# Kernel tuning notes

Measured on AMD Instinct MI355X. Metric: run time of the kernel, lower is better.

The kernel has to match this reference:

```python
import jax, jax.numpy as jnp
from jax import lax
import numpy as np

KSIZE = 3        # matching kernel size
RATE = 2         # downsample rate; raw kernel = 2*RATE = 4
FUSE_K = 3       # fusion (diagonal-sum) kernel size
SOFTMAX_SCALE = 10.0
EPS = 1e-4


def extract_patches(x, k, s, pad):
    """im2col: x [B,C,H,W] -> patches [B, L, C, k, k], L = oH*oW (row-major),
    matching torch.nn.Unfold ordering after the view/permute in the source."""
    B, C, H, W = x.shape
    xp = jnp.pad(x, ((0, 0), (0, 0), (pad, pad), (pad, pad)))
    Hp, Wp = H + 2 * pad, W + 2 * pad
    oH = (Hp - k) // s + 1
    oW = (Wp - k) // s + 1
    cols = []
    for i in range(k):
        for j in range(k):
            cols.append(xp[:, :, i:i + (oH - 1) * s + 1:s, j:j + (oW - 1) * s + 1:s])
    p = jnp.stack(cols, axis=0).reshape(k, k, B, C, oH, oW)
    return p.transpose(2, 4, 5, 3, 0, 1).reshape(B, oH * oW, C, k, k)


def fuse_diag(y, k):
    """conv2d with identity (eye(k)) kernel, 'same' padding == sum of diagonal shifts."""
    r = k // 2
    n0, n1 = y.shape
    yp = jnp.pad(y, r)
    return sum(yp[r + d:r + d + n0, r + d:r + d + n1] for d in range(-r, r + 1))


def _per_sample(xi, wi, raw_wi, mi):
    # xi: [C,Hs,Ws] downsampled foreground; wi: [L,C,3,3] bg patches;
    # raw_wi: [L,C,4,4] raw bg patches; mi: [L] patch validity mask
    C, Hs, Ws = xi.shape
    L = wi.shape[0]
    # L2-normalize each background patch (EPS added per-element inside the sum, as in source)
    wi_norm = jnp.sqrt(jnp.sum(wi * wi + EPS, axis=(1, 2, 3), keepdims=True))
    wn = (wi / wi_norm).reshape(L, -1)                      # [L, C*9]
    # correlation scores: conv2d(xi, wi_normed, pad=1) expressed as a GEMM over im2col patches
    fp = extract_patches(xi[None], KSIZE, 1, KSIZE // 2)[0].reshape(L, -1)  # [L_f, C*9]
    yi = wn @ fp.T                                          # [L_b, L_f]
    # fusion trick: identity-kernel conv along both diagonal orientations
    yi = fuse_diag(yi, FUSE_K)
    yi = yi.reshape(Hs, Ws, Hs, Ws).transpose(1, 0, 3, 2).reshape(L, L)
    yi = fuse_diag(yi, FUSE_K)
    yi = yi.reshape(Ws, Hs, Ws, Hs).transpose(1, 0, 3, 2)
    yi = yi.reshape(L, Hs, Ws)
    m = mi[:, None, None]
    yi = jax.nn.softmax(yi * m * SOFTMAX_SCALE, axis=0) * m  # softmax over bg-patch axis
    # transposed conv reconstruction with raw 4x4 patches, stride=RATE, padding=1
    k = 2 * RATE
    w_t = jnp.flip(raw_wi, (2, 3)).transpose(1, 0, 2, 3)     # [C, L, 4, 4] OIHW
    out = lax.conv_general_dilated(
        yi[None], w_t, window_strides=(1, 1),
        padding=[(k - 1 - 1, k - 1 - 1)] * 2, lhs_dilation=(RATE, RATE),
        dimension_numbers=('NCHW', 'OIHW', 'NCHW'))[0] / 4.0  # [C, H, W]
    return out


def setup_inputs() -> dict:
    key = jax.random.key(0)
    k1, k2 = jax.random.split(key)
    B, C, H, W = 4, 128, 96, 96
    b = jax.random.normal(k1, (B, C, H, W), jnp.float32)
    f = jax.random.normal(k2, (B, C, H, W), jnp.float32)
    mask = jnp.ones((B, 1, H, W), jnp.float32)
    return {"b": b, "f": f, "mask": mask}


def reference(b, f, mask):
    B, C, H, W = b.shape
    k_raw = 2 * RATE
    # raw patches from full-res background: k=4, stride=2, pad=1 (get_pad 'valid')
    raw_w = extract_patches(b, k_raw, RATE, 1)               # [B, L, C, 4, 4]
    # nearest downsample by RATE (F.interpolate nearest, scale 1/rate)
    fs = f[:, :, ::RATE, ::RATE]
    bs = b[:, :, ::RATE, ::RATE]
    Hs, Ws = fs.shape[2], fs.shape[3]
    w = extract_patches(bs, KSIZE, 1, KSIZE // 2)            # [B, L, C, 3, 3]
    ms = mask.shape[3] // Ws
    m_small = mask[:, :, ::ms, ::ms]                         # [B, 1, Hs, Ws]
    m = extract_patches(m_small, KSIZE, 1, KSIZE // 2)       # [B, L, 1, 3, 3]
    mm = (jnp.mean(m, axis=(2, 3, 4)) == 1.0).astype(jnp.float32)  # [B, L]
    y = jax.vmap(_per_sample)(fs, w, raw_w, mm)              # [B, C, H, W]
    return y
```

## Files before the change

### kernel.cpp

```cpp
#include <hip/hip_runtime.h>
#include <hip/hip_bf16.h>
#include <math.h>

#define NS   4
#define CH   128
#define HW   96
#define GS   48
#define LL   2304
#define CKN  2048
#define SCALE 10.0f
#define EPSSUM 0.1152f
#define PCH2 32
#define NCH2 72

#define S_IN  ((size_t)CH * HW * HW)
#define S_MK  ((size_t)HW * HW)
#define S_BS  ((size_t)CH * LL)
#define S_PM  ((size_t)NCH2 * LL)
#define S_BUF ((size_t)LL * LL)
#define S_W2  ((size_t)CKN * LL)
#define S_AT  ((size_t)LL * LL)

typedef __attribute__((ext_vector_type(8))) short short8;
typedef __attribute__((ext_vector_type(4))) float float4v;

#define GLDS16(gptr, lptr) \
    __builtin_amdgcn_global_load_lds((const __attribute__((address_space(1))) void*)(gptr), \
        (__attribute__((address_space(3))) void*)(lptr), 16, 0, 0)

__device__ __forceinline__ float4 ld4(const float* p) { return *reinterpret_cast<const float4*>(p); }


__global__ __launch_bounds__(256) void k_stage(const float* __restrict__ b, const float* __restrict__ f,
                                               float* __restrict__ bs_c, float* __restrict__ fs_c) {
    int s = blockIdx.z;
    b += s * S_IN; f += s * S_IN; bs_c += s * S_BS; fs_c += s * S_BS;
    int c  = blockIdx.y;
    int rs = blockIdx.x * 256 + threadIdx.x;
    int r = rs / GS, ss = rs % GS;
    int src = c * HW * HW + (2 * r) * HW + 2 * ss;
    bs_c[c * LL + rs] = b[src];
    fs_c[c * LL + rs] = f[src];
}

__global__ __launch_bounds__(256) void k_ssq(const float* __restrict__ bs_c, float* __restrict__ ssq) {
    int s = blockIdx.z;
    bs_c += s * S_BS; ssq += (size_t)s * LL;
    int rs = blockIdx.x * 256 + threadIdx.x;
    int c0 = blockIdx.y * 32;
    float acc = 0.f;
    for (int c = c0; c < c0 + 32; ++c) { float v = bs_c[c * LL + rs]; acc += v * v; }
    atomicAdd(&ssq[rs], acc);
}

__global__ __launch_bounds__(256) void k_norm_mm(const float* __restrict__ ssq, const float* __restrict__ mk,
                                                 float* __restrict__ invn, float* __restrict__ mmv) {
    int sI = blockIdx.z;
    ssq += (size_t)sI * LL; mk += sI * S_MK; invn += (size_t)sI * LL; mmv += (size_t)sI * LL;
    int p = blockIdx.x * 256 + threadIdx.x;
    int ph = p / GS, pw = p % GS;
    float acc = EPSSUM;
    float msum = 0.f;
    for (int di = -1; di <= 1; ++di)
        for (int dj = -1; dj <= 1; ++dj) {
            int r = ph + di, s = pw + dj;
            if (r >= 0 && r < GS && s >= 0 && s < GS) {
                acc  += ssq[r * GS + s];
                msum += mk[(2 * r) * HW + 2 * s];
            }
        }
    invn[p] = 1.0f / sqrtf(acc);
    mmv[p]  = (msum / 9.0f == 1.0f) ? 1.0f : 0.0f;
}

__global__ __launch_bounds__(256) void k_w2T(const float* __restrict__ b, __hip_bfloat16* __restrict__ W2T) {
    int sI = blockIdx.z;
    b += sI * S_IN; W2T += sI * S_W2;
    int ck = blockIdx.y;
    int p  = blockIdx.x * 256 + threadIdx.x;
    int c = ck >> 4, dy = (ck >> 2) & 3, dx = ck & 3;
    int ph = p / GS, pw = p % GS;
    int r = 2 * ph + dy - 1, s = 2 * pw + dx - 1;
    float v = 0.f;
    if (r >= 0 && r < HW && s >= 0 && s < HW) v = b[c * HW * HW + r * HW + s];
    W2T[(size_t)ck * LL + p] = __float2bfloat16(v);
}

__global__ __launch_bounds__(256) void k_split_T(const float* __restrict__ bs_c, const float* __restrict__ fs_c,
                                                 float* __restrict__ bufB) {
    __shared__ float tile[32][33];
    int z = blockIdx.z;
    int s = z >> 1, sel = z & 1;
    const float* X = (sel ? fs_c : bs_c) + s * S_BS;
    __hip_bfloat16* base = (__hip_bfloat16*)(bufB + s * S_BUF);
    __hip_bfloat16* hi = base + (size_t)sel * 2 * LL * CH;
    __hip_bfloat16* lo = hi + (size_t)LL * CH;
    int r0 = blockIdx.x * 32, c0 = blockIdx.y * 32;
    int tx = threadIdx.x & 31, ty = threadIdx.x >> 5;
#pragma unroll
    for (int j = 0; j < 4; ++j)
        tile[ty + 8 * j][tx] = X[(size_t)(c0 + ty + 8 * j) * LL + r0 + tx];
    __syncthreads();
#pragma unroll
    for (int j = 0; j < 4; ++j) {
        int rl = ty + 8 * j, cl = tx;
        float v = tile[cl][rl];
        __hip_bfloat16 h = __float2bfloat16(v);
        float resid = v - __bfloat162float(h);
        hi[(size_t)(r0 + rl) * CH + c0 + cl] = h;
        lo[(size_t)(r0 + rl) * CH + c0 + cl] = __float2bfloat16(resid);
    }
}

__global__ __launch_bounds__(256) void gemm1_mfma(const float* __restrict__ bufB, float* __restrict__ bufA) {
    __shared__ __hip_bfloat16 sAh[128 * 32];
    __shared__ __hip_bfloat16 sAl[128 * 32];
    __shared__ __hip_bfloat16 sBh[128 * 32];
    __shared__ __hip_bfloat16 sBl[128 * 32];
    int sI = blockIdx.z;
    const __hip_bfloat16* base = (const __hip_bfloat16*)(bufB + sI * S_BUF);
    const __hip_bfloat16* Ahi = base;
    const __hip_bfloat16* Alo = Ahi + (size_t)LL * CH;
    const __hip_bfloat16* Bhi = Alo + (size_t)LL * CH;
    const __hip_bfloat16* Blo = Bhi + (size_t)LL * CH;
    float* C = bufA + sI * S_BUF;

    int t = threadIdx.x, lane = t & 63, w = t >> 6;
    int wr = w >> 1, wc = w & 1;
    int m0 = blockIdx.y * 128, n0 = blockIdx.x * 128;

    float4v acc[4][4];
#pragma unroll
    for (int i = 0; i < 4; ++i)
#pragma unroll
        for (int j = 0; j < 4; ++j) acc[i][j] = (float4v){0.f, 0.f, 0.f, 0.f};

    for (int k0 = 0; k0 < 128; k0 += 32) {
#pragma unroll
        for (int it = 0; it < 2; ++it) {
            int chunk = it * 256 + w * 64 + lane;
            int row = chunk >> 2, ps = chunk & 3;
            int pd = ps ^ (row & 3);
            size_t ga = (size_t)(m0 + row) * 128 + k0 + pd * 8;
            size_t gb = (size_t)(n0 + row) * 128 + k0 + pd * 8;
            GLDS16(Ahi + ga, (char*)sAh + (size_t)chunk * 16);
            GLDS16(Alo + ga, (char*)sAl + (size_t)chunk * 16);
            GLDS16(Bhi + gb, (char*)sBh + (size_t)chunk * 16);
            GLDS16(Blo + gb, (char*)sBl + (size_t)chunk * 16);
        }
        __syncthreads();

        int lrow = lane & 15, part = lane >> 4;
        int sw = part ^ (lrow & 3);
        short8 ah[4], al[4], bh[4], bl[4];
#pragma unroll
        for (int i = 0; i < 4; ++i) {
            int slot = (wr * 64 + i * 16 + lrow) * 4 + sw;
            ah[i] = *reinterpret_cast<const short8*>(sAh + (size_t)slot * 8);
            al[i] = *reinterpret_cast<const short8*>(sAl + (size_t)slot * 8);
        }
#pragma unroll
        for (int j = 0; j < 4; ++j) {
            int slot = (wc * 64 + j * 16 + lrow) * 4 + sw;
            bh[j] = *reinterpret_cast<const short8*>(sBh + (size_t)slot * 8);
            bl[j] = *reinterpret_cast<const short8*>(sBl + (size_t)slot * 8);
        }
#pragma unroll
        for (int i = 0; i < 4; ++i)
#pragma unroll
            for (int j = 0; j < 4; ++j) {
                acc[i][j] = __builtin_amdgcn_mfma_f32_16x16x32_bf16(ah[i], bh[j], acc[i][j], 0, 0, 0);
                acc[i][j] = __builtin_amdgcn_mfma_f32_16x16x32_bf16(ah[i], bl[j], acc[i][j], 0, 0, 0);
                acc[i][j] = __builtin_amdgcn_mfma_f32_16x16x32_bf16(al[i], bh[j], acc[i][j], 0, 0, 0);
            }
        __syncthreads();
    }

    int col = lane & 15, rbase = (lane >> 4) * 4;
#pragma unroll
    for (int i = 0; i < 4; ++i)
#pragma unroll
        for (int j = 0; j < 4; ++j)
#pragma unroll
            for (int r = 0; r < 4; ++r) {
                int m = m0 + wr * 64 + i * 16 + rbase + r;
                int n = n0 + wc * 64 + j * 16 + col;
                C[(size_t)m * LL + n] = acc[i][j][r];
            }
}

__global__ __launch_bounds__(256) void gemm2_mfma(const __hip_bfloat16* __restrict__ attnT,
                                                  const __hip_bfloat16* __restrict__ W2T,
                                                  float* __restrict__ bufA) {
    __shared__ __hip_bfloat16 As[128 * 32];
    __shared__ __hip_bfloat16 Bs[128 * 32];
    int sI = blockIdx.z;
    const __hip_bfloat16* A = attnT + sI * S_AT;
    const __hip_bfloat16* B = W2T + sI * S_W2;
    __hip_bfloat16* C = (__hip_bfloat16*)(bufA + sI * S_BUF);

    int t = threadIdx.x;
    int lane = t & 63, w = t >> 6;
    int wr = w >> 1, wc = w & 1;
    int m0 = blockIdx.y * 128, n0 = blockIdx.x * 128;

    float4v acc[4][4];
#pragma unroll
    for (int i = 0; i < 4; ++i)
#pragma unroll
        for (int j = 0; j < 4; ++j) acc[i][j] = (float4v){0.f, 0.f, 0.f, 0.f};

    for (int k0 = 0; k0 < LL; k0 += 32) {
#pragma unroll
        for (int it = 0; it < 2; ++it) {
            int chunk = it * 256 + w * 64 + lane;
            int row = chunk >> 2, ps = chunk & 3;
            int pd = ps ^ (row & 3);
            const __hip_bfloat16* ga = A + (size_t)(m0 + row) * LL + k0 + pd * 8;
            const __hip_bfloat16* gb = B + (size_t)(n0 + row) * LL + k0 + pd * 8;
            GLDS16(ga, (char*)As + (size_t)chunk * 16);
            GLDS16(gb, (char*)Bs + (size_t)chunk * 16);
        }
        __syncthreads();

        int lrow = lane & 15, part = lane >> 4;
        int sw = part ^ (lrow & 3);
        short8 afrag[4], bfrag[4];
#pragma unroll
        for (int i = 0; i < 4; ++i) {
            int slot = (wr * 64 + i * 16 + lrow) * 4 + sw;
            afrag[i] = *reinterpret_cast<const short8*>(As + (size_t)slot * 8);
        }
#pragma unroll
        for (int j = 0; j < 4; ++j) {
            int slot = (wc * 64 + j * 16 + lrow) * 4 + sw;
            bfrag[j] = *reinterpret_cast<const short8*>(Bs + (size_t)slot * 8);
        }
#pragma unroll
        for (int i = 0; i < 4; ++i)
#pragma unroll
            for (int j = 0; j < 4; ++j)
                acc[i][j] = __builtin_amdgcn_mfma_f32_16x16x32_bf16(afrag[i], bfrag[j], acc[i][j], 0, 0, 0);
        __syncthreads();
    }

    int col = lane & 15, rbase = (lane >> 4) * 4;
#pragma unroll
    for (int i = 0; i < 4; ++i)
#pragma unroll
        for (int j = 0; j < 4; ++j)
#pragma unroll
            for (int r = 0; r < 4; ++r) {
                int m = m0 + wr * 64 + i * 16 + rbase + r;
                int n = n0 + wc * 64 + j * 16 + col;
                C[(size_t)m * CKN + n] = __float2bfloat16(acc[i][j][r]);
            }
}

__global__ __launch_bounds__(192) void k_corr_v4(const float* __restrict__ bufA, const float* __restrict__ invn,
                                                 float* __restrict__ bufB) {
    int sI = blockIdx.z;
    const float* D = bufA + sI * S_BUF;
    float* yi = bufB + sI * S_BUF;
    invn += (size_t)sI * LL;

    int p  = blockIdx.y;
    int qi = blockIdx.x * 192 + threadIdx.x;
    int q4 = qi * 4;
    int qh = q4 / GS, qw0 = q4 % GS;
    int ph = p / GS, pw = p % GS;

    float4 acc = {0.f, 0.f, 0.f, 0.f};
#pragma unroll
    for (int di = -1; di <= 1; ++di) {
        int rp = ph + di, tq = qh + di;
        if (rp < 0 || rp >= GS || tq < 0 || tq >= GS) continue;
        int r0 = rp * GS + pw;
        int c0 = tq * GS + qw0;
        {
            float4 Cc = ld4(D + (size_t)r0 * LL + c0);
            acc.x += Cc.x; acc.y += Cc.y; acc.z += Cc.z; acc.w += Cc.w;
        }
        if (pw > 0) {
            const float* rowm = D + (size_t)(r0 - 1) * LL;
            float4 L  = ld4(rowm + (qw0 > 0 ? c0 - 4 : c0));
            float4 Cm = ld4(rowm + c0);
            acc.x += (qw0 > 0 ? L.w : 0.f);
            acc.y += Cm.x; acc.z += Cm.y; acc.w += Cm.z;
        }
        if (pw < GS - 1) {
            const float* rowp = D + (size_t)(r0 + 1) * LL;
            float4 Cp = ld4(rowp + c0);
            float4 R  = ld4(rowp + (qw0 < GS - 4 ? c0 + 4 : c0));
            acc.x += Cp.y; acc.y += Cp.z; acc.z += Cp.w;
            acc.w += (qw0 < GS - 4 ? R.x : 0.f);
        }
    }
    float inv = invn[p];
    float4 outv = {inv * acc.x, inv * acc.y, inv * acc.z, inv * acc.w};
    *reinterpret_cast<float4*>(yi + (size_t)p * LL + q4) = outv;
}

__global__ __launch_bounds__(192) void k_fuse1_v4(const float* __restrict__ bufB, float* __restrict__ bufA) {
    int sI = blockIdx.z;
    const float* yi = bufB + sI * S_BUF;
    float* S1 = bufA + sI * S_BUF;
    int a  = blockIdx.y;
    int bi = blockIdx.x * 192 + threadIdx.x;
    int b4 = bi * 4;

    float4 acc = ld4(yi + (size_t)a * LL + b4);
    if (a > 0) {
        const float* rowm = yi + (size_t)(a - 1) * LL;
        float4 L  = ld4(rowm + (b4 > 0 ? b4 - 4 : b4));
        float4 Cm = ld4(rowm + b4);
        acc.x += (b4 > 0 ? L.w : 0.f);
        acc.y += Cm.x; acc.z += Cm.y; acc.w += Cm.z;
    }
    if (a < LL - 1) {
        const float* rowp = yi + (size_t)(a + 1) * LL;
        float4 Cp = ld4(rowp + b4);
        float4 R  = ld4(rowp + (b4 < LL - 4 ? b4 + 4 : b4));
        acc.x += Cp.y; acc.y += Cp.z; acc.z += Cp.w;
        acc.w += (b4 < LL - 4 ? R.x : 0.f);
    }
    *reinterpret_cast<float4*>(S1 + (size_t)a * LL + b4) = acc;
}

__device__ __forceinline__ int gmap(int x) { int hi = x / GS; int lo = x - hi * GS; return lo * GS + hi; }

__global__ __launch_bounds__(256) void k_fuse2_sm(const float* __restrict__ bufA, const float* __restrict__ mmv,
                                                  float* __restrict__ bufB,
                                                  float* __restrict__ pmax, float* __restrict__ psum) {
    int sI = blockIdx.z;
    const float* S1 = bufA + sI * S_BUF;
    float* S2 = bufB + sI * S_BUF;
    mmv += (size_t)sI * LL; pmax += sI * S_PM; psum += sI * S_PM;
    int q = blockIdx.x * 256 + threadIdx.x;
    int qh = q / GS, qw = q % GS;
    int b0 = qw * GS + qh;
    int p0 = blockIdx.y * PCH2;
    float mx = -1e30f, sm = 0.f;
    for (int i = 0; i < PCH2; ++i) {
        int p = p0 + i;
        int ph = p / GS, pw = p % GS;
        int a0 = pw * GS + ph;
        float s = 0.f;
#pragma unroll
        for (int e = -1; e <= 1; ++e) {
            int ae = a0 + e, be = b0 + e;
            if (ae >= 0 && ae < LL && be >= 0 && be < LL)
                s += S1[(size_t)gmap(ae) * LL + gmap(be)];
        }
        S2[(size_t)p * LL + q] = s;
        float lg = (mmv[p] != 0.f) ? SCALE * s : 0.f;
        float nm = fmaxf(mx, lg);
        sm = sm * __expf(mx - nm) + __expf(lg - nm);
        mx = nm;
    }
    pmax[blockIdx.y * LL + q] = mx;
    psum[blockIdx.y * LL + q] = sm;
}

__global__ __launch_bounds__(256) void k_sm2(const float* __restrict__ pmax, const float* __restrict__ psum,
                                             float* __restrict__ Mq, float* __restrict__ Dq) {
    __shared__ float red[4][64];
    int sI = blockIdx.z;
    pmax += sI * S_PM; psum += sI * S_PM; Mq += (size_t)sI * LL; Dq += (size_t)sI * LL;
    int t = threadIdx.x;
    int ql = t & 63, g = t >> 6;
    int q = blockIdx.x * 64 + ql;
    float mx = -1e30f;
    for (int ch = g * 18; ch < g * 18 + 18; ++ch) mx = fmaxf(mx, pmax[(size_t)ch * LL + q]);
    red[g][ql] = mx;
    __syncthreads();
    float mall = fmaxf(fmaxf(red[0][ql], red[1][ql]), fmaxf(red[2][ql], red[3][ql]));
    float sm = 0.f;
    for (int ch = g * 18; ch < g * 18 + 18; ++ch)
        sm += psum[(size_t)ch * LL + q] * __expf(pmax[(size_t)ch * LL + q] - mall);
    __syncthreads();
    red[g][ql] = sm;
    __syncthreads();
    if (g == 0) {
        Mq[q] = mall;
        Dq[q] = (red[0][ql] + red[1][ql]) + (red[2][ql] + red[3][ql]);
    }
}

__global__ __launch_bounds__(256) void k_sm3T(const float* __restrict__ bufB, const float* __restrict__ mmv,
                                              const float* __restrict__ Mq, const float* __restrict__ Dq,
                                              __hip_bfloat16* __restrict__ attnT) {
    __shared__ float tile[32][33];
    int sI = blockIdx.z;
    const float* S2 = bufB + sI * S_BUF;
    mmv += (size_t)sI * LL; Mq += (size_t)sI * LL; Dq += (size_t)sI * LL; attnT += sI * S_AT;
    int tx = threadIdx.x & 31, ty = threadIdx.x >> 5;
    int p0 = blockIdx.y * 32, q0 = blockIdx.x * 32;
    int q = q0 + tx;
    float mq = Mq[q], dq = Dq[q];
#pragma unroll
    for (int j = 0; j < 4; ++j) {
        int p = p0 + ty + 8 * j;
        float v = S2[(size_t)p * LL + q];
        float attn = (mmv[p] != 0.f) ? __expf(SCALE * v - mq) / dq : 0.f;
        tile[ty + 8 * j][tx] = attn;
    }
    __syncthreads();
#pragma unroll
    for (int j = 0; j < 4; ++j) {
        int qq = q0 + ty + 8 * j;
        attnT[(size_t)qq * LL + p0 + tx] = __float2bfloat16(tile[tx][ty + 8 * j]);
    }
}

__global__ __launch_bounds__(256) void k_out(const float* __restrict__ bufA, float* __restrict__ out) {
    int sI = blockIdx.z;
    const __hip_bfloat16* Z = (const __hip_bfloat16*)(bufA + sI * S_BUF);
    out += sI * S_IN;
    int c  = blockIdx.y;
    int yx = blockIdx.x * 256 + threadIdx.x;
    int y = yx / HW, x = yx % HW;
    int u = y >> 1, a = y & 1, v = x >> 1, w = x & 1;
    int qh1 = u + a - 1, qh2 = u + a, qw1 = v + w - 1, qw2 = v + w;
    int cb = c * 16;
    float s = 0.f;
    if (qh1 >= 0) {
        if (qw1 >= 0)  s += __bfloat162float(Z[(size_t)(qh1 * GS + qw1) * CKN + cb + (3 - a) * 4 + (3 - w)]);
        if (qw2 < GS)  s += __bfloat162float(Z[(size_t)(qh1 * GS + qw2) * CKN + cb + (3 - a) * 4 + (1 - w)]);
    }
    if (qh2 < GS) {
        if (qw1 >= 0)  s += __bfloat162float(Z[(size_t)(qh2 * GS + qw1) * CKN + cb + (1 - a) * 4 + (3 - w)]);
        if (qw2 < GS)  s += __bfloat162float(Z[(size_t)(qh2 * GS + qw2) * CKN + cb + (1 - a) * 4 + (1 - w)]);
    }
    out[(size_t)c * HW * HW + yx] = 0.25f * s;
}


extern "C" void kernel_launch(void* const* d_in, const int* in_sizes, int n_in,
                              void* d_out, int out_size, void* d_ws, size_t ws_size,
                              hipStream_t stream) {
    const float* b_all = (const float*)d_in[0];
    const float* f_all = (const float*)d_in[1];
    const float* m_all = (const float*)d_in[2];
    float* out = (float*)d_out;
    float* ws  = (float*)d_ws;

    const size_t perF = 2 * S_BS + 5 * (size_t)LL + 2 * S_PM + 2 * S_BUF + S_W2 / 2 + S_AT / 2;
    const size_t perB = perF * sizeof(float);
    int nb = (ws_size >= NS * perB) ? NS : ((ws_size >= 2 * perB) ? 2 : 1);

    size_t off = 0;
    float* bs_c = ws + off; off += nb * S_BS;
    float* fs_c = ws + off; off += nb * S_BS;
    float* ssq  = ws + off; off += nb * (size_t)LL;
    float* invn = ws + off; off += nb * (size_t)LL;
    float* mmv  = ws + off; off += nb * (size_t)LL;
    float* Mq   = ws + off; off += nb * (size_t)LL;
    float* Dq   = ws + off; off += nb * (size_t)LL;
    float* pmax = ws + off; off += nb * S_PM;
    float* psum = ws + off; off += nb * S_PM;
    float* bufA = ws + off; off += nb * S_BUF;
    float* bufB = ws + off; off += nb * S_BUF;
    __hip_bfloat16* W2T   = (__hip_bfloat16*)(ws + off); off += nb * S_W2 / 2;
    __hip_bfloat16* attnT = (__hip_bfloat16*)(ws + off); off += nb * S_AT / 2;

    for (int s0 = 0; s0 < NS; s0 += nb) {
        const float* b  = b_all + s0 * S_IN;
        const float* f  = f_all + s0 * S_IN;
        const float* mk = m_all + s0 * S_MK;
        float* outp = out + s0 * S_IN;

        hipMemsetAsync(ssq, 0, nb * LL * sizeof(float), stream);
        k_stage    <<<dim3(9, CH, nb), 256, 0, stream>>>(b, f, bs_c, fs_c);
        k_ssq      <<<dim3(9, 4, nb), 256, 0, stream>>>(bs_c, ssq);
        k_norm_mm  <<<dim3(9, 1, nb), 256, 0, stream>>>(ssq, mk, invn, mmv);
        k_w2T      <<<dim3(9, CKN, nb), 256, 0, stream>>>(b, W2T);
        k_split_T  <<<dim3(72, 4, 2 * nb), 256, 0, stream>>>(bs_c, fs_c, bufB);

        gemm1_mfma <<<dim3(18, 18, nb), 256, 0, stream>>>(bufB, bufA);
        k_corr_v4  <<<dim3(3, LL, nb), 192, 0, stream>>>(bufA, invn, bufB);
        k_fuse1_v4 <<<dim3(3, LL, nb), 192, 0, stream>>>(bufB, bufA);
        k_fuse2_sm <<<dim3(9, NCH2, nb), 256, 0, stream>>>(bufA, mmv, bufB, pmax, psum);

        k_sm2      <<<dim3(36, 1, nb), 256, 0, stream>>>(pmax, psum, Mq, Dq);
        k_sm3T     <<<dim3(72, 72, nb), 256, 0, stream>>>(bufB, mmv, Mq, Dq, attnT);

        gemm2_mfma <<<dim3(CKN / 128, LL / 128, nb), 256, 0, stream>>>(attnT, W2T, bufA);
        k_out      <<<dim3(36, CH, nb), 256, 0, stream>>>(bufA, outp);
    }
}
```

Baseline: 551.2 us.

## Enlarge gemm2 M-tile to 256 and vectorize second diagonal fusion pass

gemm2 now uses 256x128 block tiles, with each wave owning a 64x128 slab. This raises arithmetic intensity per LDS load and halves the grid in M. The second fusion/softmax kernel is rewritten so each thread handles four contiguous q outputs using float4 row loads of the transposed index mapping. That replaces scattered per-element gmap gathers with coalesced vector loads and explicit boundary handling. The cost is higher register pressure from 32 accumulator tiles per wave in gemm2, which could reduce occupancy.

```diff
diff --git a/kernel.cpp b/kernel.cpp
--- a/kernel.cpp
+++ b/kernel.cpp
@@ -192,7 +192,7 @@
 __global__ __launch_bounds__(256) void gemm2_mfma(const __hip_bfloat16* __restrict__ attnT,
                                                   const __hip_bfloat16* __restrict__ W2T,
                                                   float* __restrict__ bufA) {
-    __shared__ __hip_bfloat16 As[128 * 32];
+    __shared__ __hip_bfloat16 As[256 * 32];
     __shared__ __hip_bfloat16 Bs[128 * 32];
     int sI = blockIdx.z;
     const __hip_bfloat16* A = attnT + sI * S_AT;
@@ -201,45 +201,48 @@
 
     int t = threadIdx.x;
     int lane = t & 63, w = t >> 6;
-    int wr = w >> 1, wc = w & 1;
-    int m0 = blockIdx.y * 128, n0 = blockIdx.x * 128;
-
-    float4v acc[4][4];
+    int m0 = blockIdx.y * 256, n0 = blockIdx.x * 128;
+
+    float4v acc[4][8];
 #pragma unroll
     for (int i = 0; i < 4; ++i)
 #pragma unroll
-        for (int j = 0; j < 4; ++j) acc[i][j] = (float4v){0.f, 0.f, 0.f, 0.f};
+        for (int j = 0; j < 8; ++j) acc[i][j] = (float4v){0.f, 0.f, 0.f, 0.f};
 
     for (int k0 = 0; k0 < LL; k0 += 32) {
+#pragma unroll
+        for (int it = 0; it < 4; ++it) {
+            int chunk = it * 256 + w * 64 + lane;
+            int row = chunk >> 2, ps = chunk & 3;
+            int pd = ps ^ (row & 3);
+            GLDS16(A + (size_t)(m0 + row) * LL + k0 + pd * 8, (char*)As + (size_t)chunk * 16);
+        }
 #pragma unroll
         for (int it = 0; it < 2; ++it) {
             int chunk = it * 256 + w * 64 + lane;
             int row = chunk >> 2, ps = chunk & 3;
             int pd = ps ^ (row & 3);
-            const __hip_bfloat16* ga = A + (size_t)(m0 + row) * LL + k0 + pd * 8;
-            const __hip_bfloat16* gb = B + (size_t)(n0 + row) * LL + k0 + pd * 8;
-            GLDS16(ga, (char*)As + (size_t)chunk * 16);
-            GLDS16(gb, (char*)Bs + (size_t)chunk * 16);
+            GLDS16(B + (size_t)(n0 + row) * LL + k0 + pd * 8, (char*)Bs + (size_t)chunk * 16);
         }
         __syncthreads();
 
         int lrow = lane & 15, part = lane >> 4;
         int sw = part ^ (lrow & 3);
-        short8 afrag[4], bfrag[4];
+        short8 afrag[4], bfrag[8];
 #pragma unroll
         for (int i = 0; i < 4; ++i) {
-            int slot = (wr * 64 + i * 16 + lrow) * 4 + sw;
+            int slot = (w * 64 + i * 16 + lrow) * 4 + sw;
             afrag[i] = *reinterpret_cast<const short8*>(As + (size_t)slot * 8);
         }
 #pragma unroll
-        for (int j = 0; j < 4; ++j) {
-            int slot = (wc * 64 + j * 16 + lrow) * 4 + sw;
+        for (int j = 0; j < 8; ++j) {
+            int slot = (j * 16 + lrow) * 4 + sw;
             bfrag[j] = *reinterpret_cast<const short8*>(Bs + (size_t)slot * 8);
         }
 #pragma unroll
         for (int i = 0; i < 4; ++i)
 #pragma unroll
-            for (int j = 0; j < 4; ++j)
+            for (int j = 0; j < 8; ++j)
                 acc[i][j] = __builtin_amdgcn_mfma_f32_16x16x32_bf16(afrag[i], bfrag[j], acc[i][j], 0, 0, 0);
         __syncthreads();
     }
@@ -248,11 +251,11 @@
 #pragma unroll
     for (int i = 0; i < 4; ++i)
 #pragma unroll
-        for (int j = 0; j < 4; ++j)
+        for (int j = 0; j < 8; ++j)
 #pragma unroll
             for (int r = 0; r < 4; ++r) {
-                int m = m0 + wr * 64 + i * 16 + rbase + r;
-                int n = n0 + wc * 64 + j * 16 + col;
+                int m = m0 + w * 64 + i * 16 + rbase + r;
+                int n = n0 + j * 16 + col;
                 C[(size_t)m * CKN + n] = __float2bfloat16(acc[i][j][r]);
             }
 }
@@ -329,37 +332,68 @@
 
 __device__ __forceinline__ int gmap(int x) { int hi = x / GS; int lo = x - hi * GS; return lo * GS + hi; }
 
-__global__ __launch_bounds__(256) void k_fuse2_sm(const float* __restrict__ bufA, const float* __restrict__ mmv,
-                                                  float* __restrict__ bufB,
-                                                  float* __restrict__ pmax, float* __restrict__ psum) {
+__global__ __launch_bounds__(192) void k_fuse2_sm_v4(const float* __restrict__ bufA, const float* __restrict__ mmv,
+                                                     float* __restrict__ bufB,
+                                                     float* __restrict__ pmax, float* __restrict__ psum) {
     int sI = blockIdx.z;
     const float* S1 = bufA + sI * S_BUF;
     float* S2 = bufB + sI * S_BUF;
     mmv += (size_t)sI * LL; pmax += sI * S_PM; psum += sI * S_PM;
-    int q = blockIdx.x * 256 + threadIdx.x;
-    int qh = q / GS, qw = q % GS;
-    int b0 = qw * GS + qh;
+
+    int qi = blockIdx.x * 192 + threadIdx.x;
+    int q4 = qi * 4;
+    int qh = q4 / GS, qw0 = q4 % GS;
     int p0 = blockIdx.y * PCH2;
-    float mx = -1e30f, sm = 0.f;
+
+    float4 mx = {-1e30f, -1e30f, -1e30f, -1e30f};
+    float4 sm = {0.f, 0.f, 0.f, 0.f};
+
     for (int i = 0; i < PCH2; ++i) {
         int p = p0 + i;
         int ph = p / GS, pw = p % GS;
         int a0 = pw * GS + ph;
-        float s = 0.f;
+        float4 s = {0.f, 0.f, 0.f, 0.f};
 #pragma unroll
         for (int e = -1; e <= 1; ++e) {
-            int ae = a0 + e, be = b0 + e;
-            if (ae >= 0 && ae < LL && be >= 0 && be < LL)
-                s += S1[(size_t)gmap(ae) * LL + gmap(be)];
-        }
-        S2[(size_t)p * LL + q] = s;
-        float lg = (mmv[p] != 0.f) ? SCALE * s : 0.f;
-        float nm = fmaxf(mx, lg);
-        sm = sm * __expf(mx - nm) + __expf(lg - nm);
+            int ae = a0 + e;
+            if (ae < 0 || ae >= LL) continue;
+            const float* row = S1 + (size_t)gmap(ae) * LL;
+            int he = qh + e;
+            if (he >= 0 && he < GS) {
+                float4 v = ld4(row + q4 + 48 * e);
+                s.x += v.x; s.y += v.y; s.z += v.z; s.w += v.w;
+            } else if (he < 0) {
+                int base = 47 * GS + qw0;
+                float4 L  = ld4(row + (qw0 > 0 ? base - 4 : base));
+                float4 Cm = ld4(row + base);
+                s.x += (qw0 > 0 ? L.w : 0.f);
+                s.y += Cm.x; s.z += Cm.y; s.w += Cm.z;
+            } else {
+                int base = qw0;
+                float4 Cp = ld4(row + base);
+                float4 R  = ld4(row + (qw0 < GS - 4 ? base + 4 : base));
+                s.x += Cp.y; s.y += Cp.z; s.z += Cp.w;
+                s.w += (qw0 < GS - 4 ? R.x : 0.f);
+            }
+        }
+        *reinterpret_cast<float4*>(S2 + (size_t)p * LL + q4) = s;
+        bool on = (mmv[p] != 0.f);
+        float4 lg;
+        lg.x = on ? SCALE * s.x : 0.f;
+        lg.y = on ? SCALE * s.y : 0.f;
+        lg.z = on ? SCALE * s.z : 0.f;
+        lg.w = on ? SCALE * s.w : 0.f;
+        float4 nm;
+        nm.x = fmaxf(mx.x, lg.x); nm.y = fmaxf(mx.y, lg.y);
+        nm.z = fmaxf(mx.z, lg.z); nm.w = fmaxf(mx.w, lg.w);
+        sm.x = sm.x * __expf(mx.x - nm.x) + __expf(lg.x - nm.x);
+        sm.y = sm.y * __expf(mx.y - nm.y) + __expf(lg.y - nm.y);
+        sm.z = sm.z * __expf(mx.z - nm.z) + __expf(lg.z - nm.z);
+        sm.w = sm.w * __expf(mx.w - nm.w) + __expf(lg.w - nm.w);
         mx = nm;
     }
-    pmax[blockIdx.y * LL + q] = mx;
-    psum[blockIdx.y * LL + q] = sm;
+    *reinterpret_cast<float4*>(pmax + (size_t)blockIdx.y * LL + q4) = mx;
+    *reinterpret_cast<float4*>(psum + (size_t)blockIdx.y * LL + q4) = sm;
 }
 
 __global__ __launch_bounds__(256) void k_sm2(const float* __restrict__ pmax, const float* __restrict__ psum,
@@ -471,21 +505,21 @@
         float* outp = out + s0 * S_IN;
 
         hipMemsetAsync(ssq, 0, nb * LL * sizeof(float), stream);
-        k_stage    <<<dim3(9, CH, nb), 256, 0, stream>>>(b, f, bs_c, fs_c);
-        k_ssq      <<<dim3(9, 4, nb), 256, 0, stream>>>(bs_c, ssq);
-        k_norm_mm  <<<dim3(9, 1, nb), 256, 0, stream>>>(ssq, mk, invn, mmv);
-        k_w2T      <<<dim3(9, CKN, nb), 256, 0, stream>>>(b, W2T);
-        k_split_T  <<<dim3(72, 4, 2 * nb), 256, 0, stream>>>(bs_c, fs_c, bufB);
-
-        gemm1_mfma <<<dim3(18, 18, nb), 256, 0, stream>>>(bufB, bufA);
-        k_corr_v4  <<<dim3(3, LL, nb), 192, 0, stream>>>(bufA, invn, bufB);
-        k_fuse1_v4 <<<dim3(3, LL, nb), 192, 0, stream>>>(bufB, bufA);
-        k_fuse2_sm <<<dim3(9, NCH2, nb), 256, 0, stream>>>(bufA, mmv, bufB, pmax, psum);
-
-        k_sm2      <<<dim3(36, 1, nb), 256, 0, stream>>>(pmax, psum, Mq, Dq);
-        k_sm3T     <<<dim3(72, 72, nb), 256, 0, stream>>>(bufB, mmv, Mq, Dq, attnT);
-
-        gemm2_mfma <<<dim3(CKN / 128, LL / 128, nb), 256, 0, stream>>>(attnT, W2T, bufA);
-        k_out      <<<dim3(36, CH, nb), 256, 0, stream>>>(bufA, outp);
-    }
-}
+        k_stage      <<<dim3(9, CH, nb), 256, 0, stream>>>(b, f, bs_c, fs_c);
+        k_ssq        <<<dim3(9, 4, nb), 256, 0, stream>>>(bs_c, ssq);
+        k_norm_mm    <<<dim3(9, 1, nb), 256, 0, stream>>>(ssq, mk, invn, mmv);
+        k_w2T        <<<dim3(9, CKN, nb), 256, 0, stream>>>(b, W2T);
+        k_split_T    <<<dim3(72, 4, 2 * nb), 256, 0, stream>>>(bs_c, fs_c, bufB);
+
+        gemm1_mfma   <<<dim3(18, 18, nb), 256, 0, stream>>>(bufB, bufA);
+        k_corr_v4    <<<dim3(3, LL, nb), 192, 0, stream>>>(bufA, invn, bufB);
+        k_fuse1_v4   <<<dim3(3, LL, nb), 192, 0, stream>>>(bufB, bufA);
+        k_fuse2_sm_v4<<<dim3(3, NCH2, nb), 192, 0, stream>>>(bufA, mmv, bufB, pmax, psum);
+
+        k_sm2        <<<dim3(36, 1, nb), 256, 0, stream>>>(pmax, psum, Mq, Dq);
+        k_sm3T       <<<dim3(72, 72, nb), 256, 0, stream>>>(bufB, mmv, Mq, Dq, attnT);
+
+        gemm2_mfma   <<<dim3(CKN / 128, LL / 256, nb), 256, 0, stream>>>(attnT, W2T, bufA);
+        k_out        <<<dim3(36, CH, nb), 256, 0, stream>>>(bufA, outp);
+    }
+}
```

After: 645.9 us. +17.2%, slower.
